# Kernel tuning notes

Hardware: AMD Instinct MI355X
Metric: run time of the kernel (lower is better)

## Reference

```python
import jax, jax.numpy as jnp
import numpy as np

CENTER_LR = 0.5  # default center_lr in _compute_centroids_mb


def setup_inputs() -> dict:
    key = jax.random.key(0)
    k1, k2, k3 = jax.random.split(key, 3)
    N, D, K = 16384, 1024, 1024
    embedded = jax.random.normal(k1, (N, D), dtype=jnp.float32)
    centers = jax.random.normal(k2, (K, D), dtype=jnp.float32)
    count = jax.random.randint(k3, (K,), 0, 10000, dtype=jnp.int32)
    return {"embedded": embedded, "centers": centers, "count": count}


def _sq_euclidean(x, c):
    # ||x - c||^2 via expansion; avoids materializing [N, K, D]
    x2 = jnp.sum(x * x, axis=1, keepdims=True)        # [N, 1]
    c2 = jnp.sum(c * c, axis=1)[None, :]              # [1, K]
    d = x2 + c2 - 2.0 * (x @ c.T)                     # [N, K]
    return jnp.maximum(d, 0.0)


def reference(embedded, centers, count):
    N, D = embedded.shape
    K = centers.shape[0]
    # predict_hard: argmin of squared euclidean distance
    dist = _sq_euclidean(embedded, centers)           # [N, K]
    labels = jnp.argmin(dist, axis=1)                 # [N]
    # _int_to_one_hot assignment matrix
    A = jax.nn.one_hot(labels, K, dtype=embedded.dtype)  # [N, K]
    # segmented reduction: batch_cluster_sums[k] = sum_{i: label_i=k} embedded[i]
    # (embedded is detached in the original -> stop_gradient)
    batch_cluster_sums = jnp.einsum('nk,nd->kd', A, jax.lax.stop_gradient(embedded))  # [K, D]
    mask_sum = jnp.sum(A, axis=0)                     # [K]
    nonzero = mask_sum != 0                           # [K]
    # count EMA (only for clusters present in the batch)
    cc = count.astype(jnp.float32)
    cc_new = jnp.where(nonzero, (1.0 - CENTER_LR) * cc + CENTER_LR * mask_sum, cc)
    per_center_lr = 1.0 / (cc_new + 1.0)              # [K]
    batch_centers = batch_cluster_sums / jnp.where(nonzero, mask_sum, 1.0)[:, None]
    new_centers = jnp.where(
        nonzero[:, None],
        (1.0 - per_center_lr)[:, None] * centers + per_center_lr[:, None] * batch_centers,
        centers,
    )
    return new_centers
```

## Files before the change

### kernel.cpp

```cpp
#include <hip/hip_runtime.h>

typedef __attribute__((ext_vector_type(8))) short bf16x8;
typedef __attribute__((ext_vector_type(4))) float f32x4;

__device__ __forceinline__ unsigned short f2bf(float f) {
    unsigned u = __float_as_uint(f);
    unsigned r = (u + 0x7FFFu + ((u >> 16) & 1u)) >> 16;
    return (unsigned short)r;
}

__device__ __forceinline__ void gload16(const unsigned short* g, unsigned short* l) {
    __builtin_amdgcn_global_load_lds((const __attribute__((address_space(1))) void*)g,
                                     (__attribute__((address_space(3))) void*)l, 16, 0, 0);
}

#define BARRIER() do { asm volatile("" ::: "memory"); __builtin_amdgcn_s_barrier(); asm volatile("" ::: "memory"); } while (0)


__global__ void conv_x_kernel(const float* __restrict__ x, unsigned short* __restrict__ xb, int total8) {
    int i = blockIdx.x * blockDim.x + threadIdx.x;
    if (i >= total8) return;
    const float4* xv = (const float4*)x;
    float4 a = xv[(size_t)i * 2];
    float4 b = xv[(size_t)i * 2 + 1];
    uint4 o;
    o.x = (unsigned)f2bf(a.x) | ((unsigned)f2bf(a.y) << 16);
    o.y = (unsigned)f2bf(a.z) | ((unsigned)f2bf(a.w) << 16);
    o.z = (unsigned)f2bf(b.x) | ((unsigned)f2bf(b.y) << 16);
    o.w = (unsigned)f2bf(b.z) | ((unsigned)f2bf(b.w) << 16);
    ((uint4*)xb)[i] = o;
}

__global__ void conv_c_kernel(const float* __restrict__ c, unsigned short* __restrict__ cb,
                              float* __restrict__ c2, unsigned long long* __restrict__ packed,
                              int N, int D) {
    int k = blockIdx.x;
    int tid = threadIdx.x;
    const float4 v = ((const float4*)(c + (long)k * D))[tid];
    uint2 o;
    o.x = (unsigned)f2bf(v.x) | ((unsigned)f2bf(v.y) << 16);
    o.y = (unsigned)f2bf(v.z) | ((unsigned)f2bf(v.w) << 16);
    ((uint2*)(cb + (long)k * D))[tid] = o;
    float s = v.x * v.x + v.y * v.y + v.z * v.z + v.w * v.w;
    #pragma unroll
    for (int d = 1; d < 64; d <<= 1) s += __shfl_xor(s, d, 64);
    __shared__ float wsum[4];
    int lane = tid & 63, w = tid >> 6;
    if (lane == 0) wsum[w] = s;
    __syncthreads();
    if (tid == 0) c2[k] = wsum[0] + wsum[1] + wsum[2] + wsum[3];
    int gid = k * 256 + tid;
    if (gid < N) packed[gid] = ~0ull;
}

__global__ void __launch_bounds__(512, 2)
gemm_argmin_kernel(const unsigned short* __restrict__ Xb,
                   const unsigned short* __restrict__ Cb,
                   const float* __restrict__ c2,
                   unsigned long long* __restrict__ packed,
                   int D, int nt) {
    __shared__ unsigned short sh[65536];
    const int tid  = threadIdx.x;
    const int lane = tid & 63;
    const int w    = tid >> 6;
    const int wr   = w >> 2;
    const int wc   = w & 3;
    const long rowbase = (long)blockIdx.x * 256;
    const int  colbase = blockIdx.y * 256;

    const int fr = lane & 15;
    const int g  = lane >> 4;
    const int f7 = fr & 7;
    const int q0 = g ^ f7;
    const int q1 = (4 + g) ^ f7;
    const int abase0 = (wr * 128 + fr) * 64;
    const int bbase0 = 32768 + (wc * 64 + fr) * 64;

    f32x4 acc[8][4] = {};
    bf16x8 a[4][2], b[4][2];

    auto stageA = [&](int kt, int buf) {
        unsigned short* base = sh + buf * 16384;
        const unsigned short* gsrc = Xb + rowbase * D + kt * 64;
        #pragma unroll
        for (int j = 0; j < 4; ++j) {
            int c = j * 512 + w * 64 + lane;
            int r = c >> 3;
            int q = (c & 7) ^ (r & 7);
            gload16(gsrc + (long)r * D + q * 8, base + (j * 512 + w * 64) * 8);
        }
    };
    auto stageB = [&](int kt, int buf) {
        unsigned short* base = sh + 32768 + buf * 16384;
        const unsigned short* gsrc = Cb + (long)colbase * D + kt * 64;
        #pragma unroll
        for (int j = 0; j < 4; ++j) {
            int c = j * 512 + w * 64 + lane;
            int r = c >> 3;
            int q = (c & 7) ^ (r & 7);
            gload16(gsrc + (long)r * D + q * 8, base + (j * 512 + w * 64) * 8);
        }
    };

    stageA(0, 0);
    stageB(0, 0);
    asm volatile("s_waitcnt vmcnt(0)" ::: "memory");
    BARRIER();
    {
        const int bb = bbase0;
        #pragma unroll
        for (int n = 0; n < 2; ++n) {
            b[n][0] = *(const bf16x8*)&sh[bb + n * 1024 + q0 * 8];
            b[n][1] = *(const bf16x8*)&sh[bb + n * 1024 + q1 * 8];
        }
    }

    for (int t = 0; t < nt; ++t) {
        const int p  = t & 1;
        const int ab = abase0 + p * 16384;
        const int bb = bbase0 + p * 16384;
        const int bbn = bbase0 + (p ^ 1) * 16384;

        if (t < nt - 1) { stageA(t + 1, p ^ 1); stageB(t + 1, p ^ 1); }
        BARRIER();

        #pragma unroll
        for (int m = 0; m < 4; ++m) {
            a[m][0] = *(const bf16x8*)&sh[ab + m * 1024 + q0 * 8];
            a[m][1] = *(const bf16x8*)&sh[ab + m * 1024 + q1 * 8];
        }
        #pragma unroll
        for (int n = 2; n < 4; ++n) {
            b[n][0] = *(const bf16x8*)&sh[bb + n * 1024 + q0 * 8];
            b[n][1] = *(const bf16x8*)&sh[bb + n * 1024 + q1 * 8];
        }
        __builtin_amdgcn_s_setprio(1);
        #pragma unroll
        for (int m = 0; m < 4; ++m)
            #pragma unroll
            for (int n = 0; n < 2; ++n) {
                acc[m][n] = __builtin_amdgcn_mfma_f32_16x16x32_bf16(a[m][0], b[n][0], acc[m][n], 0, 0, 0);
                acc[m][n] = __builtin_amdgcn_mfma_f32_16x16x32_bf16(a[m][1], b[n][1], acc[m][n], 0, 0, 0);
            }
        __builtin_amdgcn_s_setprio(0);
        BARRIER();

        __builtin_amdgcn_s_setprio(1);
        #pragma unroll
        for (int m = 0; m < 4; ++m)
            #pragma unroll
            for (int n = 2; n < 4; ++n) {
                acc[m][n] = __builtin_amdgcn_mfma_f32_16x16x32_bf16(a[m][0], b[n][0], acc[m][n], 0, 0, 0);
                acc[m][n] = __builtin_amdgcn_mfma_f32_16x16x32_bf16(a[m][1], b[n][1], acc[m][n], 0, 0, 0);
            }
        __builtin_amdgcn_s_setprio(0);
        BARRIER();

        #pragma unroll
        for (int m = 0; m < 4; ++m) {
            a[m][0] = *(const bf16x8*)&sh[ab + (m + 4) * 1024 + q0 * 8];
            a[m][1] = *(const bf16x8*)&sh[ab + (m + 4) * 1024 + q1 * 8];
        }
        __builtin_amdgcn_s_setprio(1);
        #pragma unroll
        for (int m = 0; m < 4; ++m)
            #pragma unroll
            for (int n = 0; n < 2; ++n) {
                acc[m + 4][n] = __builtin_amdgcn_mfma_f32_16x16x32_bf16(a[m][0], b[n][0], acc[m + 4][n], 0, 0, 0);
                acc[m + 4][n] = __builtin_amdgcn_mfma_f32_16x16x32_bf16(a[m][1], b[n][1], acc[m + 4][n], 0, 0, 0);
            }
        __builtin_amdgcn_s_setprio(0);
        if (t < nt - 1) asm volatile("s_waitcnt vmcnt(0)" ::: "memory");
        BARRIER();

        if (t < nt - 1) {
            #pragma unroll
            for (int n = 0; n < 2; ++n) {
                b[n][0] = *(const bf16x8*)&sh[bbn + n * 1024 + q0 * 8];
                b[n][1] = *(const bf16x8*)&sh[bbn + n * 1024 + q1 * 8];
            }
        }
        __builtin_amdgcn_s_setprio(1);
        #pragma unroll
        for (int m = 0; m < 4; ++m)
            #pragma unroll
            for (int n = 2; n < 4; ++n) {
                acc[m + 4][n] = __builtin_amdgcn_mfma_f32_16x16x32_bf16(a[m][0], b[n][0], acc[m + 4][n], 0, 0, 0);
                acc[m + 4][n] = __builtin_amdgcn_mfma_f32_16x16x32_bf16(a[m][1], b[n][1], acc[m + 4][n], 0, 0, 0);
            }
        __builtin_amdgcn_s_setprio(0);
    }

    float c2v[4];
    int   kcol[4];
    #pragma unroll
    for (int n = 0; n < 4; ++n) {
        kcol[n] = colbase + wc * 64 + n * 16 + fr;
        c2v[n]  = c2[kcol[n]];
    }
    #pragma unroll
    for (int m = 0; m < 8; ++m) {
        #pragma unroll
        for (int reg = 0; reg < 4; ++reg) {
            unsigned long long best = ~0ull;
            #pragma unroll
            for (int n = 0; n < 4; ++n) {
                float score = c2v[n] - 2.0f * acc[m][n][reg];
                unsigned u = __float_as_uint(score);
                u ^= (u >> 31) ? 0xFFFFFFFFu : 0x80000000u;
                unsigned long long cand = ((unsigned long long)u << 32) | (unsigned)kcol[n];
                best = cand < best ? cand : best;
            }
            #pragma unroll
            for (int s = 1; s < 16; s <<= 1) {
                unsigned long long other = __shfl_xor(best, s, 64);
                best = other < best ? other : best;
            }
            if (fr == 0) {
                long row = rowbase + wr * 128 + m * 16 + g * 4 + reg;
                atomicMin(&packed[row], best);
            }
        }
    }
}

__global__ void extract16_kernel(const unsigned long long* __restrict__ p,
                                 unsigned short* __restrict__ lab, int n) {
    int i = blockIdx.x * blockDim.x + threadIdx.x;
    if (i < n) lab[i] = (unsigned short)(p[i] & 0xFFFFull);
}

__global__ void segsum_partial_kernel(const unsigned short* __restrict__ lab,
                                      const float* __restrict__ emb,
                                      float* __restrict__ partial,
                                      int* __restrict__ pcount,
                                      int N, int D) {
    const int k   = blockIdx.x;
    const int s   = blockIdx.y;
    const int tid = threadIdx.x;
    const int grp = tid >> 8;
    const int ct  = tid & 255;
    const int lane = tid & 63, w = tid >> 6;

    __shared__ int idxbuf[4096];
    __shared__ int cnts[16];
    __shared__ float4 red[4][256];

    const int slice = N >> 2;
    const int base0 = s * slice;
    int total = 0;
    for (int base = base0; base < base0 + slice; base += 1024) {
        const int n = base + tid;
        const bool m = (lab[n] == (unsigned short)k);
        const unsigned long long bal = __ballot(m);
        if (lane == 0) cnts[w] = (int)__popcll(bal);
        __syncthreads();
        int myoff = total, run = total;
        #pragma unroll
        for (int w2 = 0; w2 < 16; ++w2) {
            if (w2 == w) myoff = run;
            run += cnts[w2];
        }
        if (m) idxbuf[myoff + (int)__popcll(bal & ((1ull << lane) - 1ull))] = n;
        total = run;
        __syncthreads();
    }

    float4 acc = {0.f, 0.f, 0.f, 0.f};
    for (int j = grp; j < total; j += 4) {
        const int row = idxbuf[j];
        const float4 v = *(const float4*)(emb + (long)row * D + ct * 4);
        acc.x += v.x; acc.y += v.y; acc.z += v.z; acc.w += v.w;
    }
    red[grp][ct] = acc;
    __syncthreads();
    if (grp == 0) {
        float4 r = red[0][ct];
        #pragma unroll
        for (int q = 1; q < 4; ++q) {
            const float4 v = red[q][ct];
            r.x += v.x; r.y += v.y; r.z += v.z; r.w += v.w;
        }
        *(float4*)(partial + ((long)(k * 4 + s)) * D + ct * 4) = r;
    }
    if (tid == 0) pcount[k * 4 + s] = total;
}

__global__ void finalize_kernel(const float* __restrict__ partial,
                                const int* __restrict__ pcount,
                                const float* __restrict__ centers,
                                const int* __restrict__ cnt,
                                float* __restrict__ out, int D) {
    const int k = blockIdx.x;
    const int ct = threadIdx.x;
    float4 acc = {0.f, 0.f, 0.f, 0.f};
    int mtot = 0;
    #pragma unroll
    for (int s = 0; s < 4; ++s) {
        const float4 p = *(const float4*)(partial + ((long)(k * 4 + s)) * D + ct * 4);
        acc.x += p.x; acc.y += p.y; acc.z += p.z; acc.w += p.w;
        mtot += pcount[k * 4 + s];
    }
    const float4 cv = *(const float4*)(centers + (long)k * D + ct * 4);
    float4 o;
    if (mtot > 0) {
        float ccn = 0.5f * (float)cnt[k] + 0.5f * (float)mtot;
        float lr  = 1.0f / (ccn + 1.0f);
        float im  = 1.0f / (float)mtot;
        float om  = 1.0f - lr;
        o.x = om * cv.x + lr * (acc.x * im);
        o.y = om * cv.y + lr * (acc.y * im);
        o.z = om * cv.z + lr * (acc.z * im);
        o.w = om * cv.w + lr * (acc.w * im);
    } else {
        o = cv;
    }
    *(float4*)(out + (long)k * D + ct * 4) = o;
}


extern "C" void kernel_launch(void* const* d_in, const int* in_sizes, int n_in,
                              void* d_out, int out_size, void* d_ws, size_t ws_size,
                              hipStream_t stream) {
    const float* emb = (const float*)d_in[0];
    const float* cen = (const float*)d_in[1];
    const int*   cnt = (const int*)d_in[2];
    float* out = (float*)d_out;
    const int K = in_sizes[2];
    const int D = in_sizes[1] / K;
    const int N = in_sizes[0] / D;

    char* ws = (char*)d_ws;
    size_t xb_bytes = (size_t)N * D * 2;
    size_t cb_bytes = (size_t)K * D * 2;
    unsigned short* Xb = (unsigned short*)ws;
    unsigned short* Cb = (unsigned short*)(ws + xb_bytes);
    float* c2 = (float*)(ws + xb_bytes + cb_bytes);
    unsigned long long* packed = (unsigned long long*)(ws + xb_bytes + cb_bytes + (size_t)K * 4);
    unsigned short* lab16 = (unsigned short*)(ws + xb_bytes + cb_bytes + (size_t)K * 4 + (size_t)N * 8);
    int* pcount = (int*)(ws + xb_bytes + cb_bytes + (size_t)K * 4 + (size_t)N * 8 + (size_t)N * 2);
    float* partial = (float*)ws;

    int total8 = N * D / 8;
    conv_x_kernel<<<dim3((total8 + 255) / 256), dim3(256), 0, stream>>>(emb, Xb, total8);
    conv_c_kernel<<<dim3(K), dim3(256), 0, stream>>>(cen, Cb, c2, packed, N, D);
    gemm_argmin_kernel<<<dim3(N / 256, K / 256), dim3(512), 0, stream>>>(Xb, Cb, c2, packed, D, D / 64);
    extract16_kernel<<<dim3((N + 255) / 256), dim3(256), 0, stream>>>(packed, lab16, N);
    segsum_partial_kernel<<<dim3(K, 4), dim3(1024), 0, stream>>>(lab16, emb, partial, pcount, N, D);
    finalize_kernel<<<dim3(K), dim3(256), 0, stream>>>(partial, pcount, cen, cnt, out, D);
}
```

Measured before the change: 101.1 us.

## Reorder GEMM main loop into four-phase schedule with split A/B prefetch

Restructures the distance GEMM main loop so that each k-tile runs four MFMA quadrants in a serpentine order (A-low/B-low, A-low/B-high, A-high/B-high, A-high/B-low). The A and B global-to-LDS prefetches for the next tile are issued at different phases, each after its LDS reads. The B fragments are no longer carried across iterations, which removes the cross-iteration B preload. The aim is to spread global loads and LDS reads between MFMA clusters and reduce register pressure from holding four B fragments. The cost is an extra barrier per iteration and a changed load/compute interleaving that may expose more LDS latency.

After: 101.5 us. About the same (+0.4%).

```diff
diff --git a/kernel.cpp b/kernel.cpp
--- a/kernel.cpp
+++ b/kernel.cpp
@@ -77,7 +77,9 @@
     const int bbase0 = 32768 + (wc * 64 + fr) * 64;
 
     f32x4 acc[8][4] = {};
-    bf16x8 a[4][2], b[4][2];
+    bf16x8 aa[4][2];
+    bf16x8 bl[2][2];
+    bf16x8 bh[2][2];
 
     auto stageA = [&](int kt, int buf) {
         unsigned short* base = sh + buf * 16384;
@@ -106,89 +108,81 @@
     stageB(0, 0);
     asm volatile("s_waitcnt vmcnt(0)" ::: "memory");
     BARRIER();
-    {
-        const int bb = bbase0;
-        #pragma unroll
-        for (int n = 0; n < 2; ++n) {
-            b[n][0] = *(const bf16x8*)&sh[bb + n * 1024 + q0 * 8];
-            b[n][1] = *(const bf16x8*)&sh[bb + n * 1024 + q1 * 8];
-        }
-    }
 
     for (int t = 0; t < nt; ++t) {
         const int p  = t & 1;
         const int ab = abase0 + p * 16384;
         const int bb = bbase0 + p * 16384;
-        const int bbn = bbase0 + (p ^ 1) * 16384;
-
-        if (t < nt - 1) { stageA(t + 1, p ^ 1); stageB(t + 1, p ^ 1); }
-        BARRIER();
 
         #pragma unroll
         for (int m = 0; m < 4; ++m) {
-            a[m][0] = *(const bf16x8*)&sh[ab + m * 1024 + q0 * 8];
-            a[m][1] = *(const bf16x8*)&sh[ab + m * 1024 + q1 * 8];
-        }
-        #pragma unroll
-        for (int n = 2; n < 4; ++n) {
-            b[n][0] = *(const bf16x8*)&sh[bb + n * 1024 + q0 * 8];
-            b[n][1] = *(const bf16x8*)&sh[bb + n * 1024 + q1 * 8];
-        }
+            aa[m][0] = *(const bf16x8*)&sh[ab + m * 1024 + q0 * 8];
+            aa[m][1] = *(const bf16x8*)&sh[ab + m * 1024 + q1 * 8];
+        }
+        #pragma unroll
+        for (int n = 0; n < 2; ++n) {
+            bl[n][0] = *(const bf16x8*)&sh[bb + n * 1024 + q0 * 8];
+            bl[n][1] = *(const bf16x8*)&sh[bb + n * 1024 + q1 * 8];
+        }
+        if (t < nt - 1) stageA(t + 1, p ^ 1);
+        BARRIER();
         __builtin_amdgcn_s_setprio(1);
         #pragma unroll
         for (int m = 0; m < 4; ++m)
             #pragma unroll
             for (int n = 0; n < 2; ++n) {
-                acc[m][n] = __builtin_amdgcn_mfma_f32_16x16x32_bf16(a[m][0], b[n][0], acc[m][n], 0, 0, 0);
-                acc[m][n] = __builtin_amdgcn_mfma_f32_16x16x32_bf16(a[m][1], b[n][1], acc[m][n], 0, 0, 0);
+                acc[m][n] = __builtin_amdgcn_mfma_f32_16x16x32_bf16(aa[m][0], bl[n][0], acc[m][n], 0, 0, 0);
+                acc[m][n] = __builtin_amdgcn_mfma_f32_16x16x32_bf16(aa[m][1], bl[n][1], acc[m][n], 0, 0, 0);
             }
         __builtin_amdgcn_s_setprio(0);
         BARRIER();
 
+        #pragma unroll
+        for (int n = 0; n < 2; ++n) {
+            bh[n][0] = *(const bf16x8*)&sh[bb + (n + 2) * 1024 + q0 * 8];
+            bh[n][1] = *(const bf16x8*)&sh[bb + (n + 2) * 1024 + q1 * 8];
+        }
+        if (t < nt - 1) stageB(t + 1, p ^ 1);
+        BARRIER();
         __builtin_amdgcn_s_setprio(1);
         #pragma unroll
         for (int m = 0; m < 4; ++m)
             #pragma unroll
-            for (int n = 2; n < 4; ++n) {
-                acc[m][n] = __builtin_amdgcn_mfma_f32_16x16x32_bf16(a[m][0], b[n][0], acc[m][n], 0, 0, 0);
-                acc[m][n] = __builtin_amdgcn_mfma_f32_16x16x32_bf16(a[m][1], b[n][1], acc[m][n], 0, 0, 0);
+            for (int n = 0; n < 2; ++n) {
+                acc[m][n + 2] = __builtin_amdgcn_mfma_f32_16x16x32_bf16(aa[m][0], bh[n][0], acc[m][n + 2], 0, 0, 0);
+                acc[m][n + 2] = __builtin_amdgcn_mfma_f32_16x16x32_bf16(aa[m][1], bh[n][1], acc[m][n + 2], 0, 0, 0);
             }
         __builtin_amdgcn_s_setprio(0);
         BARRIER();
 
         #pragma unroll
         for (int m = 0; m < 4; ++m) {
-            a[m][0] = *(const bf16x8*)&sh[ab + (m + 4) * 1024 + q0 * 8];
-            a[m][1] = *(const bf16x8*)&sh[ab + (m + 4) * 1024 + q1 * 8];
-        }
+            aa[m][0] = *(const bf16x8*)&sh[ab + (m + 4) * 1024 + q0 * 8];
+            aa[m][1] = *(const bf16x8*)&sh[ab + (m + 4) * 1024 + q1 * 8];
+        }
+        BARRIER();
         __builtin_amdgcn_s_setprio(1);
         #pragma unroll
         for (int m = 0; m < 4; ++m)
             #pragma unroll
             for (int n = 0; n < 2; ++n) {
-                acc[m + 4][n] = __builtin_amdgcn_mfma_f32_16x16x32_bf16(a[m][0], b[n][0], acc[m + 4][n], 0, 0, 0);
-                acc[m + 4][n] = __builtin_amdgcn_mfma_f32_16x16x32_bf16(a[m][1], b[n][1], acc[m + 4][n], 0, 0, 0);
+                acc[m + 4][n + 2] = __builtin_amdgcn_mfma_f32_16x16x32_bf16(aa[m][0], bh[n][0], acc[m + 4][n + 2], 0, 0, 0);
+                acc[m + 4][n + 2] = __builtin_amdgcn_mfma_f32_16x16x32_bf16(aa[m][1], bh[n][1], acc[m + 4][n + 2], 0, 0, 0);
+            }
+        __builtin_amdgcn_s_setprio(0);
+        BARRIER();
+
+        __builtin_amdgcn_s_setprio(1);
+        #pragma unroll
+        for (int m = 0; m < 4; ++m)
+            #pragma unroll
+            for (int n = 0; n < 2; ++n) {
+                acc[m + 4][n] = __builtin_amdgcn_mfma_f32_16x16x32_bf16(aa[m][0], bl[n][0], acc[m + 4][n], 0, 0, 0);
+                acc[m + 4][n] = __builtin_amdgcn_mfma_f32_16x16x32_bf16(aa[m][1], bl[n][1], acc[m + 4][n], 0, 0, 0);
             }
         __builtin_amdgcn_s_setprio(0);
         if (t < nt - 1) asm volatile("s_waitcnt vmcnt(0)" ::: "memory");
         BARRIER();
-
-        if (t < nt - 1) {
-            #pragma unroll
-            for (int n = 0; n < 2; ++n) {
-                b[n][0] = *(const bf16x8*)&sh[bbn + n * 1024 + q0 * 8];
-                b[n][1] = *(const bf16x8*)&sh[bbn + n * 1024 + q1 * 8];
-            }
-        }
-        __builtin_amdgcn_s_setprio(1);
-        #pragma unroll
-        for (int m = 0; m < 4; ++m)
-            #pragma unroll
-            for (int n = 2; n < 4; ++n) {
-                acc[m + 4][n] = __builtin_amdgcn_mfma_f32_16x16x32_bf16(a[m][0], b[n][0], acc[m + 4][n], 0, 0, 0);
-                acc[m + 4][n] = __builtin_amdgcn_mfma_f32_16x16x32_bf16(a[m][1], b[n][1], acc[m + 4][n], 0, 0, 0);
-            }
-        __builtin_amdgcn_s_setprio(0);
     }
 
     float c2v[4];
```
